# Optimization experiments

Hardware: AMD Instinct MI355X
Metric: run time of the kernel (lower is better)

The kernel has to match this reference:

```python
import jax, jax.numpy as jnp
import numpy as np

Q, C, T = 256, 128, 128
L = Q + C + T            # 512
D = 1024                 # d_model
H = 8                    # heads
DK = D // H              # 128 = self_attn.d_k
F = 3                    # num_latent_relations
R = 50                   # num_relation_kinds = len(relations2id)
FF = 4 * D               # feed-forward hidden
DEFAULT_QQ_ID = 0        # relations2id['q:q-default']
EPS = 1e-5


def setup_inputs():
    key = jax.random.key(0)
    ks = jax.random.split(key, 40)
    s = 0.02
    def nrm(k, shape, scale=s):
        return jax.random.normal(k, shape, jnp.float32) * scale
    inp = {
        'x': jax.random.normal(ks[0], (1, L, D), jnp.float32),
        'qc_relation': jax.random.uniform(ks[1], (Q, C, F), jnp.float32),
        'cq_relation': jax.random.uniform(ks[2], (C, Q, F), jnp.float32),
        'qt_relation': jax.random.uniform(ks[3], (Q, T, F), jnp.float32),
        'tq_relation': jax.random.uniform(ks[4], (T, Q, F), jnp.float32),
        'ct_relation': jax.random.randint(ks[5], (C + T, C + T), 0, R, jnp.int32),
        'predefined_relation': jax.random.randint(ks[6], (L, L), 0, R, jnp.int32),
        'mask': jnp.ones((1, L, L), jnp.int32),
        # relation embedding tables
        'rel_k_emb': nrm(ks[7], (R, DK)), 'rel_v_emb': nrm(ks[8], (R, DK)),
        'lqc_k': nrm(ks[9], (F, DK)), 'lqc_v': nrm(ks[10], (F, DK)),
        'lcq_k': nrm(ks[11], (F, DK)), 'lcq_v': nrm(ks[12], (F, DK)),
        'lqt_k': nrm(ks[13], (F, DK)), 'lqt_v': nrm(ks[14], (F, DK)),
        'ltq_k': nrm(ks[15], (F, DK)), 'ltq_v': nrm(ks[16], (F, DK)),
        # attention projections (torch Linear: y = x @ W.T + b)
        'Wq': nrm(ks[17], (D, D)), 'bq': jnp.zeros((D,), jnp.float32),
        'Wk': nrm(ks[18], (D, D)), 'bk': jnp.zeros((D,), jnp.float32),
        'Wv': nrm(ks[19], (D, D)), 'bv': jnp.zeros((D,), jnp.float32),
        'Wo': nrm(ks[20], (D, D)), 'bo': jnp.zeros((D,), jnp.float32),
        # layer norms
        'ln1_g': jnp.ones((D,), jnp.float32), 'ln1_b': jnp.zeros((D,), jnp.float32),
        'ln2_g': jnp.ones((D,), jnp.float32), 'ln2_b': jnp.zeros((D,), jnp.float32),
        # FFN
        'W1': nrm(ks[21], (FF, D)), 'b1': jnp.zeros((FF,), jnp.float32),
        'W2': nrm(ks[22], (D, FF)), 'b2': jnp.zeros((D,), jnp.float32),
    }
    return inp


def layer_norm(x, g, b):
    m = jnp.mean(x, -1, keepdims=True)
    v = jnp.mean((x - m) ** 2, -1, keepdims=True)
    return (x - m) * jax.lax.rsqrt(v + EPS) * g + b


def build_latent_relation(ct, qc, cq, qt, tq, emb, lqc, lcq, lqt, ltq):
    # qq block: every entry is the default-qq embedding row
    qq = jnp.broadcast_to(emb[DEFAULT_QQ_ID], (Q, Q, DK))
    qc_e = jnp.einsum('qcf,fd->qcd', qc, lqc)
    cq_e = jnp.einsum('cqf,fd->cqd', cq, lcq)
    qt_e = jnp.einsum('qtf,fd->qtd', qt, lqt)
    tq_e = jnp.einsum('tqf,fd->tqd', tq, ltq)
    ct_e = emb[ct]                                      # [(c+t),(c+t),DK]
    top = jnp.concatenate([qq, qc_e, qt_e], axis=1)      # [Q, L, DK]
    bot = jnp.concatenate([jnp.concatenate([cq_e, tq_e], 0), ct_e], axis=1)  # [C+T, L, DK]
    return jnp.concatenate([top, bot], axis=0)           # [L, L, DK]


def relation_attention(x, rel_k, rel_v, mask, Wq, bq, Wk, bk, Wv, bv, Wo, bo):
    B = x.shape[0]
    def proj(W, b):
        return (x @ W.T + b).reshape(B, L, H, DK).transpose(0, 2, 1, 3)  # [B,H,L,DK]
    q, k, v = proj(Wq, bq), proj(Wk, bk), proj(Wv, bv)
    scores = (jnp.einsum('bhid,bhjd->bhij', q, k)
              + jnp.einsum('bhid,ijd->bhij', q, rel_k)) / jnp.sqrt(jnp.float32(DK))
    scores = jnp.where(mask[:, None] == 0, jnp.float32(-1e9), scores)
    p = jax.nn.softmax(scores, axis=-1)
    o = (jnp.einsum('bhij,bhjd->bhid', p, v)
         + jnp.einsum('bhij,ijd->bhid', p, rel_v))
    o = o.transpose(0, 2, 1, 3).reshape(B, L, D)
    return o @ Wo.T + bo


def reference(x, qc_relation, cq_relation, qt_relation, tq_relation,
              ct_relation, predefined_relation, mask,
              rel_k_emb, rel_v_emb, lqc_k, lqc_v, lcq_k, lcq_v,
              lqt_k, lqt_v, ltq_k, ltq_v,
              Wq, bq, Wk, bk, Wv, bv, Wo, bo,
              ln1_g, ln1_b, ln2_g, ln2_b, W1, b1, W2, b2):
    # latent relation build + combine with predefined lookup
    rel_k = (rel_k_emb[predefined_relation]
             + build_latent_relation(ct_relation, qc_relation, cq_relation,
                                     qt_relation, tq_relation,
                                     rel_k_emb, lqc_k, lcq_k, lqt_k, ltq_k))
    rel_v = (rel_v_emb[predefined_relation]
             + build_latent_relation(ct_relation, qc_relation, cq_relation,
                                     qt_relation, tq_relation,
                                     rel_v_emb, lqc_v, lcq_v, lqt_v, ltq_v))
    # sublayer 0: pre-norm relation-biased self attention (dropout=0)
    h = x + relation_attention(layer_norm(x, ln1_g, ln1_b), rel_k, rel_v, mask,
                               Wq, bq, Wk, bk, Wv, bv, Wo, bo)
    # sublayer 1: pre-norm FFN
    y = layer_norm(h, ln2_g, ln2_b)
    ffn = jax.nn.relu(y @ W1.T + b1) @ W2.T + b2
    return h + ffn
```

## Files before the change

### kernel.cpp

```cpp
#include <hip/hip_runtime.h>
#include <hip/hip_bf16.h>

#define LL 512
#define DD 1024
#define HH 8
#define DKK 128
#define QQ 256
#define CCC 128
#define TTT 128
#define RR 50
#define FFF 4096
#define KLD 576
#define SLD 576
#define PLD 1152

typedef __attribute__((ext_vector_type(8))) short short8;
typedef __attribute__((ext_vector_type(4))) float float4v;

__device__ __forceinline__ unsigned short f2bu(float f) {
  __hip_bfloat16 h = __float2bfloat16(f);
  unsigned short u; __builtin_memcpy(&u, &h, 2); return u;
}
__device__ __forceinline__ float b2f(unsigned short u) {
  unsigned int v = ((unsigned int)u) << 16;
  float f; __builtin_memcpy(&f, &v, 4); return f;
}
__device__ __forceinline__ int4 cvt8(float4 x, float4 y) {
  int4 o;
  o.x = (int)f2bu(x.x) | ((int)f2bu(x.y) << 16);
  o.y = (int)f2bu(x.z) | ((int)f2bu(x.w) << 16);
  o.z = (int)f2bu(y.x) | ((int)f2bu(y.y) << 16);
  o.w = (int)f2bu(y.z) | ((int)f2bu(y.w) << 16);
  return o;
}

__device__ __forceinline__ void lds_barrier() {
  __builtin_amdgcn_sched_barrier(0);
  __builtin_amdgcn_s_waitcnt(0xC07F);
  __builtin_amdgcn_s_barrier();
  __builtin_amdgcn_sched_barrier(0);
}

#define LOADSET(A0,A1,B0,B1,F0,F1,F2,F3,itv) { int k0v = (itv) << 6;          \
  A0 = *(const int4*)(Az + (size_t)(bm + r)*lda + k0v + gc*8);                \
  A1 = *(const int4*)(Az + (size_t)(bm + 32 + r)*lda + k0v + gc*8);           \
  if constexpr (!CONVB) {                                                     \
    B0 = *(const int4*)(Bz16 + (size_t)(bnb + r)*ldb + k0v + gc*8);           \
    if constexpr (NB > 1)                                                     \
      B1 = *(const int4*)(Bz16 + (size_t)(bnb + 32 + r)*ldb + k0v + gc*8);    \
  } else {                                                                    \
    F0 = *(const float4*)(Bz32 + (size_t)(bnb + r)*ldb + k0v + gc*8);         \
    F1 = *(const float4*)(Bz32 + (size_t)(bnb + r)*ldb + k0v + gc*8 + 4);     \
    if constexpr (NB > 1) {                                                   \
      F2 = *(const float4*)(Bz32 + (size_t)(bnb + 32 + r)*ldb + k0v + gc*8);  \
      F3 = *(const float4*)(Bz32 + (size_t)(bnb + 32 + r)*ldb + k0v + gc*8 + 4); } } }

#define STORESET2(basep,A0,A1,B0,B1,F0,F1,F2,F3) {                            \
  char* bse = (basep);                                                        \
  *(int4*)(bse + r*128 + sl*16) = A0;                                         \
  *(int4*)(bse + (32 + r)*128 + sl*16) = A1;                                  \
  if constexpr (!CONVB) {                                                     \
    *(int4*)(bse + ABYTES + r*128 + sl*16) = B0;                              \
    if constexpr (NB > 1)                                                     \
      *(int4*)(bse + ABYTES + (32 + r)*128 + sl*16) = B1;                     \
  } else {                                                                    \
    *(int4*)(bse + ABYTES + r*128 + sl*16) = cvt8(F0, F1);                    \
    if constexpr (NB > 1)                                                     \
      *(int4*)(bse + ABYTES + (32 + r)*128 + sl*16) = cvt8(F2, F3); } }

__global__ __launch_bounds__(256) void kprep_kernel(
    const float* __restrict__ embk,
    const float* __restrict__ lqc, const float* __restrict__ lqt,
    const float* __restrict__ lcq, const float* __restrict__ ltq,
    unsigned short* __restrict__ Kh)
{
  int g = blockIdx.x*256 + threadIdx.x;
  if (g >= 8*64*128) return;
  int d = g & 127, rr = (g >> 7) & 63, h = g >> 13;
  float v = 0.f;
  if (rr < 50) v = embk[rr*128 + d];
  else if (rr < 62) {
    int u = rr - 50; int tb = u/3, f = u - tb*3;
    const float* tab = (tb==0) ? lqc : (tb==1) ? lqt : (tb==2) ? lcq : ltq;
    v = tab[f*128 + d];
  }
  Kh[((size_t)h*KLD + 512 + rr)*DKK + d] = f2bu(v);
}

__global__ __launch_bounds__(256) void ln_bf16_kernel(const float* __restrict__ x,
    const float* __restrict__ g, const float* __restrict__ b,
    unsigned short* __restrict__ y)
{
  int row = blockIdx.x, t = threadIdx.x;
  const float4 xv = ((const float4*)(x + row*DD))[t];
  float s  = xv.x+xv.y+xv.z+xv.w;
  float ss = xv.x*xv.x+xv.y*xv.y+xv.z*xv.z+xv.w*xv.w;
  __shared__ float rs[256], rss[256];
  rs[t]=s; rss[t]=ss; __syncthreads();
  for (int st=128; st>0; st>>=1){ if (t<st){ rs[t]+=rs[t+st]; rss[t]+=rss[t+st]; } __syncthreads(); }
  float mean = rs[0] * (1.0f/DD);
  float var  = rss[0]*(1.0f/DD) - mean*mean;
  float inv  = rsqrtf(var + 1e-5f);
  float4 gv = ((const float4*)g)[t], bv = ((const float4*)b)[t];
  ushort4 ov;
  ov.x = f2bu((xv.x-mean)*inv*gv.x + bv.x);
  ov.y = f2bu((xv.y-mean)*inv*gv.y + bv.y);
  ov.z = f2bu((xv.z-mean)*inv*gv.z + bv.z);
  ov.w = f2bu((xv.w-mean)*inv*gv.w + bv.w);
  ((ushort4*)(y + row*DD))[t] = ov;
}

__global__ __launch_bounds__(256) void ln_bf16_addb_kernel(float* __restrict__ x,
    const float* __restrict__ g, const float* __restrict__ b,
    const float* __restrict__ b2, unsigned short* __restrict__ y)
{
  int row = blockIdx.x, t = threadIdx.x;
  const float4 xv = ((const float4*)(x + row*DD))[t];
  float s  = xv.x+xv.y+xv.z+xv.w;
  float ss = xv.x*xv.x+xv.y*xv.y+xv.z*xv.z+xv.w*xv.w;
  __shared__ float rs[256], rss[256];
  rs[t]=s; rss[t]=ss; __syncthreads();
  for (int st=128; st>0; st>>=1){ if (t<st){ rs[t]+=rs[t+st]; rss[t]+=rss[t+st]; } __syncthreads(); }
  float mean = rs[0] * (1.0f/DD);
  float var  = rss[0]*(1.0f/DD) - mean*mean;
  float inv  = rsqrtf(var + 1e-5f);
  float4 gv = ((const float4*)g)[t], bv = ((const float4*)b)[t];
  ushort4 ov;
  ov.x = f2bu((xv.x-mean)*inv*gv.x + bv.x);
  ov.y = f2bu((xv.y-mean)*inv*gv.y + bv.y);
  ov.z = f2bu((xv.z-mean)*inv*gv.z + bv.z);
  ov.w = f2bu((xv.w-mean)*inv*gv.w + bv.w);
  ((ushort4*)(y + row*DD))[t] = ov;
  float4 b2v = ((const float4*)b2)[t];
  float4 nx; nx.x = xv.x+b2v.x; nx.y = xv.y+b2v.y; nx.z = xv.z+b2v.z; nx.w = xv.w+b2v.w;
  ((float4*)(x + row*DD))[t] = nx;
}

template<int BN, int DEPTH, int CONVB, int ZK, int OUT_BF16, int RELU, int HAS_SRC, int HAS_BIAS>
__global__ __launch_bounds__(256) void gemm_pl(
    const unsigned short* __restrict__ A, int lda, size_t sAz,
    const void* __restrict__ Bv, int ldb, size_t sBz,
    const float* __restrict__ bias,
    const float* __restrict__ src, int ldsrc, size_t sSz,
    void* __restrict__ Cv, int ldc, size_t sCz,
    int K)
{
  constexpr int BM = 64;
  constexpr int WM = 32, WN = BN/2, FM = 2, FN = WN/16;
  constexpr int NB = BN/32;
  constexpr int ABYTES = BM*128, TILE = ABYTES + BN*128;
  __shared__ char lds[2*TILE];
  int t = threadIdx.x, w = t >> 6, l = t & 63;
  size_t z = blockIdx.z;
  const unsigned short* Az = A + z*sAz;
  const unsigned short* Bz16 = (const unsigned short*)Bv + (CONVB ? 0 : z*sBz);
  const float*          Bz32 = (const float*)Bv + (CONVB ? z*sBz : 0);
  int bm = blockIdx.y*BM, bn = blockIdx.x*BN;
  int bnb = bn;
  int wm = (w>>1)*WM, wn = (w&1)*WN;

  float4v acc[FM][FN];
  #pragma unroll
  for (int m=0;m<FM;++m)
    #pragma unroll
    for (int n=0;n<FN;++n) acc[m][n] = (float4v){0.f,0.f,0.f,0.f};

  int r = t >> 3, sl = t & 7;
  int gc = sl ^ (r & 7);
  int quad = l >> 4, lrow = l & 15;
  const int nit = K >> 6;

  int4 Aa0, Aa1, Ab0, Ab1;  float4 Af0, Af1, Af2, Af3;
  int4 Ba0, Ba1, Bb0, Bb1;  float4 Bf0, Bf1, Bf2, Bf3;
  int4 Ca0, Ca1, Cb0, Cb1;  float4 Cf0, Cf1, Cf2, Cf3;
  int4 Da0, Da1, Db0, Db1;  float4 Df0, Df1, Df2, Df3;

  auto compute = [&](const char* base) {
    const char* ab = base;
    const char* bb = base + ABYTES;
    #pragma unroll
    for (int step=0; step<2; ++step) {
      int c = step*4 + quad;
      short8 af[FM], bf[FN];
      #pragma unroll
      for (int m=0;m<FM;++m) {
        int Rw = wm + m*16 + lrow;
        af[m] = *(const short8*)(ab + Rw*128 + ((c ^ (Rw & 7))*16));
      }
      #pragma unroll
      for (int n=0;n<FN;++n) {
        int Rw = wn + n*16 + lrow;
        bf[n] = *(const short8*)(bb + Rw*128 + ((c ^ (Rw & 7))*16));
      }
      #pragma unroll
      for (int m=0;m<FM;++m)
        #pragma unroll
        for (int n=0;n<FN;++n)
          acc[m][n] = __builtin_amdgcn_mfma_f32_16x16x32_bf16(af[m], bf[n], acc[m][n], 0, 0, 0);
    }
  };

  if constexpr (DEPTH == 2) {
    LOADSET(Aa0,Aa1,Ab0,Ab1,Af0,Af1,Af2,Af3, 0);
    LOADSET(Ba0,Ba1,Bb0,Bb1,Bf0,Bf1,Bf2,Bf3, 1);
    for (int it = 0; it < nit; it += 2) {
      STORESET2(lds, Aa0,Aa1,Ab0,Ab1,Af0,Af1,Af2,Af3);
      if (it + 2 < nit) LOADSET(Aa0,Aa1,Ab0,Ab1,Af0,Af1,Af2,Af3, it+2);
      lds_barrier();
      compute(lds);
      STORESET2(lds + TILE, Ba0,Ba1,Bb0,Bb1,Bf0,Bf1,Bf2,Bf3);
      if (it + 3 < nit) LOADSET(Ba0,Ba1,Bb0,Bb1,Bf0,Bf1,Bf2,Bf3, it+3);
      lds_barrier();
      compute(lds + TILE);
    }
  } else {
    LOADSET(Aa0,Aa1,Ab0,Ab1,Af0,Af1,Af2,Af3, 0);
    LOADSET(Ba0,Ba1,Bb0,Bb1,Bf0,Bf1,Bf2,Bf3, 1);
    LOADSET(Ca0,Ca1,Cb0,Cb1,Cf0,Cf1,Cf2,Cf3, 2);
    LOADSET(Da0,Da1,Db0,Db1,Df0,Df1,Df2,Df3, 3);
    for (int it = 0; it < nit; it += 4) {
      STORESET2(lds, Aa0,Aa1,Ab0,Ab1,Af0,Af1,Af2,Af3);
      if (it + 4 < nit) LOADSET(Aa0,Aa1,Ab0,Ab1,Af0,Af1,Af2,Af3, it+4);
      lds_barrier();
      compute(lds);
      STORESET2(lds + TILE, Ba0,Ba1,Bb0,Bb1,Bf0,Bf1,Bf2,Bf3);
      if (it + 5 < nit) LOADSET(Ba0,Ba1,Bb0,Bb1,Bf0,Bf1,Bf2,Bf3, it+5);
      lds_barrier();
      compute(lds + TILE);
      STORESET2(lds, Ca0,Ca1,Cb0,Cb1,Cf0,Cf1,Cf2,Cf3);
      if (it + 6 < nit) LOADSET(Ca0,Ca1,Cb0,Cb1,Cf0,Cf1,Cf2,Cf3, it+6);
      lds_barrier();
      compute(lds);
      STORESET2(lds + TILE, Da0,Da1,Db0,Db1,Df0,Df1,Df2,Df3);
      if (it + 7 < nit) LOADSET(Da0,Da1,Db0,Db1,Df0,Df1,Df2,Df3, it+7);
      lds_barrier();
      compute(lds + TILE);
    }
  }

  #pragma unroll
  for (int m=0;m<FM;++m)
    #pragma unroll
    for (int n=0;n<FN;++n)
      #pragma unroll
      for (int rg=0;rg<4;++rg) {
        int row = bm + wm + m*16 + quad*4 + rg;
        int col = bn + wn + n*16 + lrow;
        float vv = acc[m][n][rg];
        if (ZK) {
          atomicAdd(&((float*)Cv)[(size_t)row*ldc + col], vv);
        } else {
          if (HAS_BIAS) vv += bias[col];
          if (HAS_SRC)  vv += src[z*sSz + (size_t)row*ldsrc + col];
          if (RELU) vv = fmaxf(vv, 0.f);
          if (OUT_BF16) ((unsigned short*)Cv)[z*sCz + (size_t)row*ldc + col] = f2bu(vv);
          else          ((float*)Cv)[z*sCz + (size_t)row*ldc + col] = vv;
        }
      }
}

__global__ __launch_bounds__(256) void gemm_qkv_pl(
    const unsigned short* __restrict__ A,
    const float* __restrict__ Wq, const float* __restrict__ Wk,
    const float* __restrict__ Wv,
    const float* __restrict__ bq, const float* __restrict__ bk,
    const float* __restrict__ bv,
    unsigned short* __restrict__ Qh, unsigned short* __restrict__ Kh,
    unsigned short* __restrict__ Vt)
{
  constexpr int BN = 64, CONVB = 1;
  constexpr int WM = 32, WN = 32, FM = 2, FN = 2;
  constexpr int NB = 2;
  constexpr int ABYTES = 64*128, TILE = ABYTES + BN*128;
  __shared__ char lds[2*TILE];
  int t = threadIdx.x, w = t >> 6, l = t & 63;
  int bm = blockIdx.y*64, bn = blockIdx.x*BN;
  int wm = (w>>1)*WM, wn = (w&1)*WN;
  const int lda = DD, ldb = DD, nit = DD >> 6;
  const unsigned short* Az = A;
  int part0 = bn >> 10;
  const float* Bz32 = (part0==0 ? Wq : part0==1 ? Wk : Wv) + (size_t)(bn & 1023)*DD;
  const unsigned short* Bz16 = nullptr; (void)Bz16;
  int bnb = 0;

  float4v acc[FM][FN];
  #pragma unroll
  for (int m=0;m<FM;++m)
    #pragma unroll
    for (int n=0;n<FN;++n) acc[m][n] = (float4v){0.f,0.f,0.f,0.f};

  int r = t >> 3, sl = t & 7;
  int gc = sl ^ (r & 7);
  int quad = l >> 4, lrow = l & 15;

  int4 Aa0, Aa1, Ab0, Ab1;  float4 Af0, Af1, Af2, Af3;
  int4 Ba0, Ba1, Bb0, Bb1;  float4 Bf0, Bf1, Bf2, Bf3;
  int4 Ca0, Ca1, Cb0, Cb1;  float4 Cf0, Cf1, Cf2, Cf3;
  int4 Da0, Da1, Db0, Db1;  float4 Df0, Df1, Df2, Df3;

  auto compute = [&](const char* base) {
    const char* ab = base;
    const char* bb = base + ABYTES;
    #pragma unroll
    for (int step=0; step<2; ++step) {
      int c = step*4 + quad;
      short8 af[FM], bf[FN];
      #pragma unroll
      for (int m=0;m<FM;++m) {
        int Rw = wm + m*16 + lrow;
        af[m] = *(const short8*)(ab + Rw*128 + ((c ^ (Rw & 7))*16));
      }
      #pragma unroll
      for (int n=0;n<FN;++n) {
        int Rw = wn + n*16 + lrow;
        bf[n] = *(const short8*)(bb + Rw*128 + ((c ^ (Rw & 7))*16));
      }
      #pragma unroll
      for (int m=0;m<FM;++m)
        #pragma unroll
        for (int n=0;n<FN;++n)
          acc[m][n] = __builtin_amdgcn_mfma_f32_16x16x32_bf16(af[m], bf[n], acc[m][n], 0, 0, 0);
    }
  };

  LOADSET(Aa0,Aa1,Ab0,Ab1,Af0,Af1,Af2,Af3, 0);
  LOADSET(Ba0,Ba1,Bb0,Bb1,Bf0,Bf1,Bf2,Bf3, 1);
  LOADSET(Ca0,Ca1,Cb0,Cb1,Cf0,Cf1,Cf2,Cf3, 2);
  LOADSET(Da0,Da1,Db0,Db1,Df0,Df1,Df2,Df3, 3);
  for (int it = 0; it < nit; it += 4) {
    STORESET2(lds, Aa0,Aa1,Ab0,Ab1,Af0,Af1,Af2,Af3);
    if (it + 4 < nit) LOADSET(Aa0,Aa1,Ab0,Ab1,Af0,Af1,Af2,Af3, it+4);
    lds_barrier();
    compute(lds);
    STORESET2(lds + TILE, Ba0,Ba1,Bb0,Bb1,Bf0,Bf1,Bf2,Bf3);
    if (it + 5 < nit) LOADSET(Ba0,Ba1,Bb0,Bb1,Bf0,Bf1,Bf2,Bf3, it+5);
    lds_barrier();
    compute(lds + TILE);
    STORESET2(lds, Ca0,Ca1,Cb0,Cb1,Cf0,Cf1,Cf2,Cf3);
    if (it + 6 < nit) LOADSET(Ca0,Ca1,Cb0,Cb1,Cf0,Cf1,Cf2,Cf3, it+6);
    lds_barrier();
    compute(lds);
    STORESET2(lds + TILE, Da0,Da1,Db0,Db1,Df0,Df1,Df2,Df3);
    if (it + 7 < nit) LOADSET(Da0,Da1,Db0,Db1,Df0,Df1,Df2,Df3, it+7);
    lds_barrier();
    compute(lds + TILE);
  }

  #pragma unroll
  for (int m=0;m<FM;++m)
    #pragma unroll
    for (int n=0;n<FN;++n)
      #pragma unroll
      for (int rg=0;rg<4;++rg) {
        int row = bm + wm + m*16 + quad*4 + rg;
        int col = bn + wn + n*16 + lrow;
        int part = col >> 10, hh = (col >> 7) & 7, d = col & 127;
        const float* bp = (part==0) ? bq : (part==1) ? bk : bv;
        float vv = acc[m][n][rg] + bp[col & 1023];
        unsigned short o = f2bu(vv);
        if (part == 0)      Qh[((size_t)hh*LL + row)*DKK + d] = o;
        else if (part == 1) Kh[((size_t)hh*KLD + row)*DKK + d] = o;
        else                Vt[((size_t)hh*DKK + d)*LL + row] = o;
      }
}

__global__ __launch_bounds__(512) void softmax_pw_kernel(
    float* __restrict__ S,
    const float* __restrict__ qcr, const float* __restrict__ cqr,
    const float* __restrict__ qtr, const float* __restrict__ tqr,
    const int* __restrict__ ct,   const int* __restrict__ pred,
    const int* __restrict__ mask,
    const float* __restrict__ embv,
    const float* __restrict__ lqc_v, const float* __restrict__ lcq_v,
    const float* __restrict__ lqt_v, const float* __restrict__ ltq_v,
    float* __restrict__ o2)
{
  int i = blockIdx.x, j = threadIdx.x, w = j >> 6;
  __shared__ float qerow8[8][52];
  __shared__ float lq1s[8][3], lq2s[8][3];
  __shared__ float pws[8][52];
  __shared__ float pf1s[8][3], pf2s[8][3];
  __shared__ float redm[8][8], reds[8][8];

  for (int k = j; k < 8*52; k += 512) ((float*)pws)[k] = 0.f;
  if (j < 24) { ((float*)pf1s)[j] = 0.f; ((float*)pf2s)[j] = 0.f; }
  if (j < 400) {
    int h = j / 50, rr = j - h*50;
    qerow8[h][rr] = S[((size_t)(h*LL + i))*SLD + 512 + rr];
  } else if (j >= 448 && j < 472) {
    int u = j - 448; int h = u / 3, f = u - h*3;
    int base = (i < QQ) ? 562 : (i < QQ+CCC) ? 568 : 571;
    lq1s[h][f] = S[((size_t)(h*LL + i))*SLD + base + f];
    lq2s[h][f] = (i < QQ) ? S[((size_t)(h*LL + i))*SLD + 565 + f] : 0.f;
  }

  int predv = pred[i*LL + j];
  int maskv = mask[i*LL + j];
  float c0=0.f, c1=0.f, c2=0.f; int route; int scat2 = 0;
  if (i < QQ) {
    if (j < QQ) { route = 0; scat2 = 0; }
    else if (j < QQ+CCC) { const float* rr = qcr + (i*CCC + (j-QQ))*3;
      c0=rr[0]; c1=rr[1]; c2=rr[2]; route = 1; }
    else { const float* rr = qtr + (i*TTT + (j-QQ-CCC))*3;
      c0=rr[0]; c1=rr[1]; c2=rr[2]; route = 2; }
  } else {
    if (j < QQ) { const float* rr = (i < QQ+CCC) ? cqr + ((i-QQ)*QQ + j)*3
                                                 : tqr + ((i-QQ-CCC)*QQ + j)*3;
      c0=rr[0]; c1=rr[1]; c2=rr[2]; route = 1; }
    else { route = 0; scat2 = ct[(i-QQ)*(CCC+TTT) + (j-QQ)]; }
  }

  float sv[8];
  #pragma unroll
  for (int h=0; h<8; ++h) sv[h] = S[((size_t)(h*LL + i))*SLD + j];
  __syncthreads();

  #pragma unroll
  for (int h=0; h<8; ++h) {
    float s = sv[h] + qerow8[h][predv];
    if (route == 0)      s += qerow8[h][scat2];
    else if (route == 1) s += c0*lq1s[h][0] + c1*lq1s[h][1] + c2*lq1s[h][2];
    else                 s += c0*lq2s[h][0] + c1*lq2s[h][1] + c2*lq2s[h][2];
    s *= 0.08838834764831845f;
    if (maskv == 0) s = -1e9f;
    sv[h] = s;
  }

  float mv[8];
  #pragma unroll
  for (int h=0; h<8; ++h) mv[h] = sv[h];
  #pragma unroll
  for (int off=32; off>=1; off>>=1) {
    #pragma unroll
    for (int h=0; h<8; ++h) mv[h] = fmaxf(mv[h], __shfl_xor(mv[h], off));
  }
  if ((j & 63) == 0) {
    #pragma unroll
    for (int h=0; h<8; ++h) redm[h][w] = mv[h];
  }
  __syncthreads();
  float ev[8];
  #pragma unroll
  for (int h=0; h<8; ++h) {
    float mx = redm[h][0];
    #pragma unroll
    for (int k=1; k<8; ++k) mx = fmaxf(mx, redm[h][k]);
    ev[h] = __expf(sv[h] - mx);
  }
  float sm[8];
  #pragma unroll
  for (int h=0; h<8; ++h) sm[h] = ev[h];
  #pragma unroll
  for (int off=32; off>=1; off>>=1) {
    #pragma unroll
    for (int h=0; h<8; ++h) sm[h] += __shfl_xor(sm[h], off);
  }
  if ((j & 63) == 0) {
    #pragma unroll
    for (int h=0; h<8; ++h) reds[h][w] = sm[h];
  }
  __syncthreads();
  float pv[8];
  #pragma unroll
  for (int h=0; h<8; ++h) {
    float tot = 0.f;
    #pragma unroll
    for (int k=0; k<8; ++k) tot += reds[h][k];
    pv[h] = ev[h] * (1.0f/tot);
    ((unsigned short*)S)[((size_t)(h*LL + i))*PLD + j] = f2bu(pv[h]);
    atomicAdd(&pws[h][predv], pv[h]);
    if (route == 0) atomicAdd(&pws[h][scat2], pv[h]);
  }
  if (route == 1) {
    #pragma unroll
    for (int h=0; h<8; ++h) {
      float f0 = pv[h]*c0, f1 = pv[h]*c1, f2 = pv[h]*c2;
      #pragma unroll
      for (int off=32; off>=1; off>>=1) {
        f0 += __shfl_xor(f0, off); f1 += __shfl_xor(f1, off); f2 += __shfl_xor(f2, off);
      }
      if ((j & 63) == 0) {
        atomicAdd(&pf1s[h][0], f0); atomicAdd(&pf1s[h][1], f1); atomicAdd(&pf1s[h][2], f2);
      }
    }
  } else if (route == 2) {
    #pragma unroll
    for (int h=0; h<8; ++h) {
      float f0 = pv[h]*c0, f1 = pv[h]*c1, f2 = pv[h]*c2;
      #pragma unroll
      for (int off=32; off>=1; off>>=1) {
        f0 += __shfl_xor(f0, off); f1 += __shfl_xor(f1, off); f2 += __shfl_xor(f2, off);
      }
      if ((j & 63) == 0) {
        atomicAdd(&pf2s[h][0], f0); atomicAdd(&pf2s[h][1], f1); atomicAdd(&pf2s[h][2], f2);
      }
    }
  }
  __syncthreads();

  {
    int h0 = j >> 7;
    int d  = j & 127;
    const float* tab1; const float* tab2 = nullptr;
    if (i < QQ)          { tab1 = lqc_v; tab2 = lqt_v; }
    else if (i < QQ+CCC) { tab1 = lcq_v; }
    else                 { tab1 = ltq_v; }
    float accA = 0.f, accB = 0.f;
    #pragma unroll 5
    for (int rr = 0; rr < RR; ++rr) {
      float evv = embv[rr*128 + d];
      accA += pws[h0][rr]*evv; accB += pws[h0+4][rr]*evv;
    }
    float t0 = tab1[d], t1 = tab1[128+d], t2 = tab1[256+d];
    accA += pf1s[h0][0]*t0 + pf1s[h0][1]*t1 + pf1s[h0][2]*t2;
    accB += pf1s[h0+4][0]*t0 + pf1s[h0+4][1]*t1 + pf1s[h0+4][2]*t2;
    if (tab2) {
      float u0 = tab2[d], u1 = tab2[128+d], u2 = tab2[256+d];
      accA += pf2s[h0][0]*u0 + pf2s[h0][1]*u1 + pf2s[h0][2]*u2;
      accB += pf2s[h0+4][0]*u0 + pf2s[h0+4][1]*u1 + pf2s[h0+4][2]*u2;
    }
    o2[((size_t)(h0*LL) + i)*DKK + d] = accA;
    o2[((size_t)((h0+4)*LL) + i)*DKK + d] = accB;
  }
}

extern "C" void kernel_launch(void* const* d_in, const int* in_sizes, int n_in,
                              void* d_out, int out_size, void* d_ws, size_t ws_size,
                              hipStream_t stream)
{
  const float* x    = (const float*)d_in[0];
  const float* qcr  = (const float*)d_in[1];
  const float* cqr  = (const float*)d_in[2];
  const float* qtr  = (const float*)d_in[3];
  const float* tqr  = (const float*)d_in[4];
  const int*   ct   = (const int*)d_in[5];
  const int*   pred = (const int*)d_in[6];
  const int*   mask = (const int*)d_in[7];
  const float* embk = (const float*)d_in[8];
  const float* embv = (const float*)d_in[9];
  const float* lqc_k = (const float*)d_in[10];
  const float* lqc_v = (const float*)d_in[11];
  const float* lcq_k = (const float*)d_in[12];
  const float* lcq_v = (const float*)d_in[13];
  const float* lqt_k = (const float*)d_in[14];
  const float* lqt_v = (const float*)d_in[15];
  const float* ltq_k = (const float*)d_in[16];
  const float* ltq_v = (const float*)d_in[17];
  const float* Wq = (const float*)d_in[18]; const float* bq = (const float*)d_in[19];
  const float* Wk = (const float*)d_in[20]; const float* bk = (const float*)d_in[21];
  const float* Wv = (const float*)d_in[22]; const float* bv = (const float*)d_in[23];
  const float* Wo = (const float*)d_in[24]; const float* bo = (const float*)d_in[25];
  const float* ln1_g = (const float*)d_in[26]; const float* ln1_b = (const float*)d_in[27];
  const float* ln2_g = (const float*)d_in[28]; const float* ln2_b = (const float*)d_in[29];
  const float* W1 = (const float*)d_in[30]; const float* b1 = (const float*)d_in[31];
  const float* W2 = (const float*)d_in[32]; const float* b2 = (const float*)d_in[33];
  float* out = (float*)d_out;

  float* wsf = (float*)d_ws;
  float* S    = wsf;
  float* o2   = S + (size_t)HH*LL*SLD;
  unsigned short* ub = (unsigned short*)(o2 + (size_t)HH*LL*DKK);
  unsigned short* ybuf_b = ub;
  unsigned short* obuf_b = ybuf_b + LL*DD;
  unsigned short* Qh     = obuf_b + LL*DD;
  unsigned short* Kh     = Qh + (size_t)HH*LL*DKK;
  unsigned short* Vt     = Kh + (size_t)HH*KLD*DKK;
  unsigned short* PS     = (unsigned short*)S;
  unsigned short* hidden = (unsigned short*)S;

  kprep_kernel<<<(8*64*128 + 255)/256, 256, 0, stream>>>(
      embk, lqc_k, lqt_k, lcq_k, ltq_k, Kh);
  ln_bf16_kernel<<<LL, 256, 0, stream>>>(x, ln1_g, ln1_b, ybuf_b);
  gemm_qkv_pl<<<dim3(48, 8), 256, 0, stream>>>(ybuf_b, Wq, Wk, Wv, bq, bk, bv,
                                               Qh, Kh, Vt);
  gemm_pl<64,2,0,0,0,0,0,0><<<dim3(9, 8, 8), 256, 0, stream>>>(
      Qh, DKK, (size_t)LL*DKK, Kh, DKK, (size_t)KLD*DKK,
      nullptr, nullptr, 0, 0, S, SLD, (size_t)LL*SLD, DKK);
  softmax_pw_kernel<<<LL, 512, 0, stream>>>(
      S, qcr, cqr, qtr, tqr, ct, pred, mask,
      embv, lqc_v, lcq_v, lqt_v, ltq_v, o2);
  gemm_pl<32,4,0,0,1,0,1,0><<<dim3(4, 8, 8), 256, 0, stream>>>(
      PS, PLD, (size_t)LL*PLD, Vt, LL, (size_t)DKK*LL,
      nullptr, o2, DKK, (size_t)LL*DKK, obuf_b, DD, (size_t)DKK, LL);
  gemm_pl<32,4,1,0,0,0,1,1><<<dim3(32, 8, 1), 256, 0, stream>>>(
      obuf_b, DD, 0, Wo, DD, 0, bo, x, DD, 0, out, DD, 0, DD);
  ln_bf16_addb_kernel<<<LL, 256, 0, stream>>>(out, ln2_g, ln2_b, b2, ybuf_b);
  gemm_pl<64,4,1,0,1,1,0,1><<<dim3(64, 8, 1), 256, 0, stream>>>(
      ybuf_b, DD, 0, W1, DD, 0, b1, nullptr, 0, 0, hidden, FFF, 0, DD);
  gemm_pl<64,4,1,1,0,0,0,0><<<dim3(16, 8, 4), 256, 0, stream>>>(
      hidden, FFF, (size_t)1024, W2, FFF, (size_t)1024,
      nullptr, nullptr, 0, 0, out, DD, 0, 1024);
}
```

Before: 251.8 us.

## Fuse QK^T, relation-biased softmax, and PV into one attention kernel

Replaces three launches (QK^T GEMM, softmax with relation scatter, PV GEMM) with a single kernel. Each block handles 16 query rows of one head, computes the scores into LDS with MFMA, applies the relation biases and softmax, and accumulates the relation-value terms. It then multiplies P by V from LDS and writes bf16 output directly. This removes the global round-trips for S, P and o2 plus two launches, but the grid is only 256 blocks with large LDS use, which may lower occupancy.

```diff
diff --git a/kernel.cpp b/kernel.cpp
--- a/kernel.cpp
+++ b/kernel.cpp
@@ -12,7 +12,6 @@
 #define FFF 4096
 #define KLD 576
 #define SLD 576
-#define PLD 1152
 
 typedef __attribute__((ext_vector_type(8))) short short8;
 typedef __attribute__((ext_vector_type(4))) float float4v;
@@ -364,163 +363,229 @@
       }
 }
 
-__global__ __launch_bounds__(512) void softmax_pw_kernel(
-    float* __restrict__ S,
+#define AT_QROWB 272
+#define AT_KROWB 272
+#define AT_SROW  584
+#define AT_PROWB 1040
+#define AT_VROWB 144
+#define AT_OFF_KT 4352
+#define AT_OFF_S  21760
+#define AT_OFF_V  21760
+#define AT_OFF_PW 59136
+#define AT_OFF_PF1 62464
+#define AT_OFF_PF2 62720
+#define AT_LDS 62976
+
+__global__ __launch_bounds__(256) void attn_fused(
+    const unsigned short* __restrict__ Qh, const unsigned short* __restrict__ Kh,
+    const unsigned short* __restrict__ Vt,
     const float* __restrict__ qcr, const float* __restrict__ cqr,
     const float* __restrict__ qtr, const float* __restrict__ tqr,
-    const int* __restrict__ ct,   const int* __restrict__ pred,
+    const int* __restrict__ ct, const int* __restrict__ pred,
     const int* __restrict__ mask,
-    const float* __restrict__ embv,
-    const float* __restrict__ lqc_v, const float* __restrict__ lcq_v,
-    const float* __restrict__ lqt_v, const float* __restrict__ ltq_v,
-    float* __restrict__ o2)
+    const float* __restrict__ embv, const float* __restrict__ lqc_v,
+    const float* __restrict__ lcq_v, const float* __restrict__ lqt_v,
+    const float* __restrict__ ltq_v,
+    unsigned short* __restrict__ obuf)
 {
-  int i = blockIdx.x, j = threadIdx.x, w = j >> 6;
-  __shared__ float qerow8[8][52];
-  __shared__ float lq1s[8][3], lq2s[8][3];
-  __shared__ float pws[8][52];
-  __shared__ float pf1s[8][3], pf2s[8][3];
-  __shared__ float redm[8][8], reds[8][8];
-
-  for (int k = j; k < 8*52; k += 512) ((float*)pws)[k] = 0.f;
-  if (j < 24) { ((float*)pf1s)[j] = 0.f; ((float*)pf2s)[j] = 0.f; }
-  if (j < 400) {
-    int h = j / 50, rr = j - h*50;
-    qerow8[h][rr] = S[((size_t)(h*LL + i))*SLD + 512 + rr];
-  } else if (j >= 448 && j < 472) {
-    int u = j - 448; int h = u / 3, f = u - h*3;
-    int base = (i < QQ) ? 562 : (i < QQ+CCC) ? 568 : 571;
-    lq1s[h][f] = S[((size_t)(h*LL + i))*SLD + base + f];
-    lq2s[h][f] = (i < QQ) ? S[((size_t)(h*LL + i))*SLD + 565 + f] : 0.f;
-  }
-
-  int predv = pred[i*LL + j];
-  int maskv = mask[i*LL + j];
-  float c0=0.f, c1=0.f, c2=0.f; int route; int scat2 = 0;
-  if (i < QQ) {
-    if (j < QQ) { route = 0; scat2 = 0; }
-    else if (j < QQ+CCC) { const float* rr = qcr + (i*CCC + (j-QQ))*3;
-      c0=rr[0]; c1=rr[1]; c2=rr[2]; route = 1; }
-    else { const float* rr = qtr + (i*TTT + (j-QQ-CCC))*3;
-      c0=rr[0]; c1=rr[1]; c2=rr[2]; route = 2; }
-  } else {
-    if (j < QQ) { const float* rr = (i < QQ+CCC) ? cqr + ((i-QQ)*QQ + j)*3
-                                                 : tqr + ((i-QQ-CCC)*QQ + j)*3;
-      c0=rr[0]; c1=rr[1]; c2=rr[2]; route = 1; }
-    else { route = 0; scat2 = ct[(i-QQ)*(CCC+TTT) + (j-QQ)]; }
-  }
-
-  float sv[8];
-  #pragma unroll
-  for (int h=0; h<8; ++h) sv[h] = S[((size_t)(h*LL + i))*SLD + j];
-  __syncthreads();
-
-  #pragma unroll
-  for (int h=0; h<8; ++h) {
-    float s = sv[h] + qerow8[h][predv];
-    if (route == 0)      s += qerow8[h][scat2];
-    else if (route == 1) s += c0*lq1s[h][0] + c1*lq1s[h][1] + c2*lq1s[h][2];
-    else                 s += c0*lq2s[h][0] + c1*lq2s[h][1] + c2*lq2s[h][2];
+  __shared__ __align__(16) char lds[AT_LDS];
+  const int t = threadIdx.x;
+  const int w = t >> 6, l = t & 63, quad = l >> 4, lrow = l & 15;
+  const int i0 = blockIdx.x * 16, h = blockIdx.y;
+
+  for (int k2 = t; k2 < 960; k2 += 256) ((float*)(lds + AT_OFF_PW))[k2] = 0.f;
+
+  {
+    int qr = t >> 4, qc = t & 15;
+    *(int4*)(lds + qr*AT_QROWB + qc*16) =
+        *(const int4*)(Qh + ((size_t)h*LL + i0 + qr)*DKK + qc*8);
+  }
+
+  const int kr = t >> 4, kc = t & 15;
+  int4 kv0, kv1, kv2, kv3;
+#define AT_LOADK(jtv) { size_t kb = (size_t)h*KLD + (size_t)(jtv)*64 + kr;     \
+    kv0 = *(const int4*)(Kh + (kb     )*DKK + kc*8);                           \
+    kv1 = *(const int4*)(Kh + (kb + 16)*DKK + kc*8);                           \
+    kv2 = *(const int4*)(Kh + (kb + 32)*DKK + kc*8);                           \
+    kv3 = *(const int4*)(Kh + (kb + 48)*DKK + kc*8); }
+#define AT_STOREK() {                                                          \
+    *(int4*)(lds + AT_OFF_KT + (kr     )*AT_KROWB + kc*16) = kv0;              \
+    *(int4*)(lds + AT_OFF_KT + (kr + 16)*AT_KROWB + kc*16) = kv1;              \
+    *(int4*)(lds + AT_OFF_KT + (kr + 32)*AT_KROWB + kc*16) = kv2;              \
+    *(int4*)(lds + AT_OFF_KT + (kr + 48)*AT_KROWB + kc*16) = kv3; }
+
+  AT_LOADK(0);
+  for (int jt = 0; jt < 9; ++jt) {
+    lds_barrier();
+    AT_STOREK();
+    if (jt + 1 < 9) AT_LOADK(jt + 1);
+    lds_barrier();
+    float4v acc = (float4v){0.f,0.f,0.f,0.f};
+    #pragma unroll
+    for (int kk = 0; kk < 4; ++kk) {
+      int c = kk*4 + quad;
+      short8 af = *(const short8*)(lds + lrow*AT_QROWB + c*16);
+      short8 bf = *(const short8*)(lds + AT_OFF_KT + (w*16 + lrow)*AT_KROWB + c*16);
+      acc = __builtin_amdgcn_mfma_f32_16x16x32_bf16(af, bf, acc, 0, 0, 0);
+    }
+    #pragma unroll
+    for (int rg = 0; rg < 4; ++rg)
+      ((float*)(lds + AT_OFF_S))[(quad*4 + rg)*AT_SROW + jt*64 + w*16 + lrow] = acc[rg];
+  }
+  lds_barrier();
+
+  const int row = t >> 4, l16 = t & 15;
+  const int i = i0 + row;
+  const float* Srow = (const float*)(lds + AT_OFF_S) + row*AT_SROW;
+  const int base = (i0 < QQ) ? 562 : (i0 < QQ + CCC) ? 568 : 571;
+  const float lq1a = Srow[base], lq1b = Srow[base+1], lq1c = Srow[base+2];
+  const float lq2a = Srow[565], lq2b = Srow[566], lq2c = Srow[567];
+
+  const int vr = t >> 3, vc = t & 7;
+  int4 vv0, vv1, vv2, vv3;
+#define AT_LOADV(itv) { size_t vb = (size_t)h*DKK + vr;                        \
+    size_t vo = (size_t)(itv)*64 + vc*8;                                       \
+    vv0 = *(const int4*)(Vt + (vb      )*LL + vo);                             \
+    vv1 = *(const int4*)(Vt + (vb + 32)*LL + vo);                              \
+    vv2 = *(const int4*)(Vt + (vb + 64)*LL + vo);                              \
+    vv3 = *(const int4*)(Vt + (vb + 96)*LL + vo); }
+#define AT_STOREV() {                                                          \
+    *(int4*)(lds + AT_OFF_V + (vr     )*AT_VROWB + vc*16) = vv0;               \
+    *(int4*)(lds + AT_OFF_V + (vr + 32)*AT_VROWB + vc*16) = vv1;               \
+    *(int4*)(lds + AT_OFF_V + (vr + 64)*AT_VROWB + vc*16) = vv2;               \
+    *(int4*)(lds + AT_OFF_V + (vr + 96)*AT_VROWB + vc*16) = vv3; }
+  AT_LOADV(0);
+
+  float sv[32];
+  #pragma unroll
+  for (int m = 0; m < 32; ++m) {
+    int j = m*16 + l16;
+    int predv = pred[i*LL + j];
+    int maskv = mask[i*LL + j];
+    float s = Srow[j] + Srow[512 + predv];
+    if (i0 < QQ) {
+      if (j < QQ) s += Srow[512];
+      else if (j < QQ + CCC) {
+        const float* r3 = qcr + ((size_t)i*CCC + (j - QQ))*3;
+        s += r3[0]*lq1a + r3[1]*lq1b + r3[2]*lq1c;
+      } else {
+        const float* r3 = qtr + ((size_t)i*TTT + (j - QQ - CCC))*3;
+        s += r3[0]*lq2a + r3[1]*lq2b + r3[2]*lq2c;
+      }
+    } else {
+      if (j < QQ) {
+        const float* r3 = (i < QQ + CCC) ? cqr + ((size_t)(i - QQ)*QQ + j)*3
+                                         : tqr + ((size_t)(i - QQ - CCC)*QQ + j)*3;
+        s += r3[0]*lq1a + r3[1]*lq1b + r3[2]*lq1c;
+      } else {
+        int scat2 = ct[(i - QQ)*(CCC + TTT) + (j - QQ)];
+        s += Srow[512 + scat2];
+      }
+    }
     s *= 0.08838834764831845f;
     if (maskv == 0) s = -1e9f;
-    sv[h] = s;
-  }
-
-  float mv[8];
-  #pragma unroll
-  for (int h=0; h<8; ++h) mv[h] = sv[h];
-  #pragma unroll
-  for (int off=32; off>=1; off>>=1) {
-    #pragma unroll
-    for (int h=0; h<8; ++h) mv[h] = fmaxf(mv[h], __shfl_xor(mv[h], off));
-  }
-  if ((j & 63) == 0) {
-    #pragma unroll
-    for (int h=0; h<8; ++h) redm[h][w] = mv[h];
-  }
-  __syncthreads();
-  float ev[8];
-  #pragma unroll
-  for (int h=0; h<8; ++h) {
-    float mx = redm[h][0];
-    #pragma unroll
-    for (int k=1; k<8; ++k) mx = fmaxf(mx, redm[h][k]);
-    ev[h] = __expf(sv[h] - mx);
-  }
-  float sm[8];
-  #pragma unroll
-  for (int h=0; h<8; ++h) sm[h] = ev[h];
-  #pragma unroll
-  for (int off=32; off>=1; off>>=1) {
-    #pragma unroll
-    for (int h=0; h<8; ++h) sm[h] += __shfl_xor(sm[h], off);
-  }
-  if ((j & 63) == 0) {
-    #pragma unroll
-    for (int h=0; h<8; ++h) reds[h][w] = sm[h];
-  }
-  __syncthreads();
-  float pv[8];
-  #pragma unroll
-  for (int h=0; h<8; ++h) {
-    float tot = 0.f;
-    #pragma unroll
-    for (int k=0; k<8; ++k) tot += reds[h][k];
-    pv[h] = ev[h] * (1.0f/tot);
-    ((unsigned short*)S)[((size_t)(h*LL + i))*PLD + j] = f2bu(pv[h]);
-    atomicAdd(&pws[h][predv], pv[h]);
-    if (route == 0) atomicAdd(&pws[h][scat2], pv[h]);
-  }
-  if (route == 1) {
-    #pragma unroll
-    for (int h=0; h<8; ++h) {
-      float f0 = pv[h]*c0, f1 = pv[h]*c1, f2 = pv[h]*c2;
-      #pragma unroll
-      for (int off=32; off>=1; off>>=1) {
-        f0 += __shfl_xor(f0, off); f1 += __shfl_xor(f1, off); f2 += __shfl_xor(f2, off);
-      }
-      if ((j & 63) == 0) {
-        atomicAdd(&pf1s[h][0], f0); atomicAdd(&pf1s[h][1], f1); atomicAdd(&pf1s[h][2], f2);
-      }
-    }
-  } else if (route == 2) {
-    #pragma unroll
-    for (int h=0; h<8; ++h) {
-      float f0 = pv[h]*c0, f1 = pv[h]*c1, f2 = pv[h]*c2;
-      #pragma unroll
-      for (int off=32; off>=1; off>>=1) {
-        f0 += __shfl_xor(f0, off); f1 += __shfl_xor(f1, off); f2 += __shfl_xor(f2, off);
-      }
-      if ((j & 63) == 0) {
-        atomicAdd(&pf2s[h][0], f0); atomicAdd(&pf2s[h][1], f1); atomicAdd(&pf2s[h][2], f2);
-      }
-    }
-  }
-  __syncthreads();
-
-  {
-    int h0 = j >> 7;
-    int d  = j & 127;
-    const float* tab1; const float* tab2 = nullptr;
-    if (i < QQ)          { tab1 = lqc_v; tab2 = lqt_v; }
-    else if (i < QQ+CCC) { tab1 = lcq_v; }
-    else                 { tab1 = ltq_v; }
-    float accA = 0.f, accB = 0.f;
+    sv[m] = s;
+  }
+  float mx = sv[0];
+  #pragma unroll
+  for (int m = 1; m < 32; ++m) mx = fmaxf(mx, sv[m]);
+  #pragma unroll
+  for (int off = 8; off >= 1; off >>= 1) mx = fmaxf(mx, __shfl_xor(mx, off));
+  float sum = 0.f;
+  #pragma unroll
+  for (int m = 0; m < 32; ++m) { float e = __expf(sv[m] - mx); sv[m] = e; sum += e; }
+  #pragma unroll
+  for (int off = 8; off >= 1; off >>= 1) sum += __shfl_xor(sum, off);
+  const float inv = 1.0f / sum;
+
+  float f0=0.f, f1=0.f, f2=0.f, g0=0.f, g1=0.f, g2=0.f;
+  #pragma unroll
+  for (int m = 0; m < 32; ++m) {
+    int j = m*16 + l16;
+    float p = sv[m] * inv;
+    *(unsigned short*)(lds + row*AT_PROWB + j*2) = f2bu(p);
+    int predv = pred[i*LL + j];
+    atomicAdd((float*)(lds + AT_OFF_PW) + row*52 + predv, p);
+    if (i0 < QQ) {
+      if (j < QQ) atomicAdd((float*)(lds + AT_OFF_PW) + row*52, p);
+      else if (j < QQ + CCC) {
+        const float* r3 = qcr + ((size_t)i*CCC + (j - QQ))*3;
+        f0 += p*r3[0]; f1 += p*r3[1]; f2 += p*r3[2];
+      } else {
+        const float* r3 = qtr + ((size_t)i*TTT + (j - QQ - CCC))*3;
+        g0 += p*r3[0]; g1 += p*r3[1]; g2 += p*r3[2];
+      }
+    } else {
+      if (j < QQ) {
+        const float* r3 = (i < QQ + CCC) ? cqr + ((size_t)(i - QQ)*QQ + j)*3
+                                         : tqr + ((size_t)(i - QQ - CCC)*QQ + j)*3;
+        f0 += p*r3[0]; f1 += p*r3[1]; f2 += p*r3[2];
+      } else {
+        int scat2 = ct[(i - QQ)*(CCC + TTT) + (j - QQ)];
+        atomicAdd((float*)(lds + AT_OFF_PW) + row*52 + scat2, p);
+      }
+    }
+  }
+  #pragma unroll
+  for (int off = 8; off >= 1; off >>= 1) {
+    f0 += __shfl_xor(f0, off); f1 += __shfl_xor(f1, off); f2 += __shfl_xor(f2, off);
+    g0 += __shfl_xor(g0, off); g1 += __shfl_xor(g1, off); g2 += __shfl_xor(g2, off);
+  }
+  if (l16 == 0) {
+    float* pf1 = (float*)(lds + AT_OFF_PF1) + row*4;
+    float* pf2 = (float*)(lds + AT_OFF_PF2) + row*4;
+    pf1[0] = f0; pf1[1] = f1; pf1[2] = f2;
+    pf2[0] = g0; pf2[1] = g1; pf2[2] = g2;
+  }
+
+  float4v oacc0 = (float4v){0.f,0.f,0.f,0.f};
+  float4v oacc1 = (float4v){0.f,0.f,0.f,0.f};
+  for (int it = 0; it < 8; ++it) {
+    lds_barrier();
+    AT_STOREV();
+    if (it + 1 < 8) AT_LOADV(it + 1);
+    lds_barrier();
+    #pragma unroll
+    for (int kk = 0; kk < 2; ++kk) {
+      int c = kk*4 + quad;
+      short8 pa = *(const short8*)(lds + lrow*AT_PROWB + it*128 + c*16);
+      short8 vf0 = *(const short8*)(lds + AT_OFF_V + (w*32 + lrow)*AT_VROWB + c*16);
+      short8 vf1 = *(const short8*)(lds + AT_OFF_V + (w*32 + 16 + lrow)*AT_VROWB + c*16);
+      oacc0 = __builtin_amdgcn_mfma_f32_16x16x32_bf16(pa, vf0, oacc0, 0, 0, 0);
+      oacc1 = __builtin_amdgcn_mfma_f32_16x16x32_bf16(pa, vf1, oacc1, 0, 0, 0);
+    }
+  }
+
+  const float* tab1 = (i0 < QQ) ? lqc_v : (i0 < QQ + CCC) ? lcq_v : ltq_v;
+  const bool hasT2 = (i0 < QQ);
+  const float* pws = (const float*)(lds + AT_OFF_PW);
+  #pragma unroll
+  for (int n = 0; n < 2; ++n) {
+    int d = w*32 + n*16 + lrow;
+    float a0=0.f, a1=0.f, a2=0.f, a3=0.f;
     #pragma unroll 5
     for (int rr = 0; rr < RR; ++rr) {
-      float evv = embv[rr*128 + d];
-      accA += pws[h0][rr]*evv; accB += pws[h0+4][rr]*evv;
-    }
-    float t0 = tab1[d], t1 = tab1[128+d], t2 = tab1[256+d];
-    accA += pf1s[h0][0]*t0 + pf1s[h0][1]*t1 + pf1s[h0][2]*t2;
-    accB += pf1s[h0+4][0]*t0 + pf1s[h0+4][1]*t1 + pf1s[h0+4][2]*t2;
-    if (tab2) {
-      float u0 = tab2[d], u1 = tab2[128+d], u2 = tab2[256+d];
-      accA += pf2s[h0][0]*u0 + pf2s[h0][1]*u1 + pf2s[h0][2]*u2;
-      accB += pf2s[h0+4][0]*u0 + pf2s[h0+4][1]*u1 + pf2s[h0+4][2]*u2;
-    }
-    o2[((size_t)(h0*LL) + i)*DKK + d] = accA;
-    o2[((size_t)((h0+4)*LL) + i)*DKK + d] = accB;
+      float evv = embv[rr*DKK + d];
+      a0 += pws[(quad*4+0)*52 + rr]*evv;
+      a1 += pws[(quad*4+1)*52 + rr]*evv;
+      a2 += pws[(quad*4+2)*52 + rr]*evv;
+      a3 += pws[(quad*4+3)*52 + rr]*evv;
+    }
+    float t0 = tab1[d], t1 = tab1[DKK + d], t2 = tab1[2*DKK + d];
+    float u0 = 0.f, u1 = 0.f, u2 = 0.f;
+    if (hasT2) { u0 = lqt_v[d]; u1 = lqt_v[DKK + d]; u2 = lqt_v[2*DKK + d]; }
+    #pragma unroll
+    for (int rg = 0; rg < 4; ++rg) {
+      int rw = quad*4 + rg;
+      const float* pf1 = (const float*)(lds + AT_OFF_PF1) + rw*4;
+      const float* pf2 = (const float*)(lds + AT_OFF_PF2) + rw*4;
+      float aval = (rg==0) ? a0 : (rg==1) ? a1 : (rg==2) ? a2 : a3;
+      float oval = (n==0) ? oacc0[rg] : oacc1[rg];
+      float val = oval + aval
+                + pf1[0]*t0 + pf1[1]*t1 + pf1[2]*t2
+                + pf2[0]*u0 + pf2[1]*u1 + pf2[2]*u2;
+      obuf[(size_t)(i0 + rw)*DD + h*DKK + d] = f2bu(val);
+    }
   }
 }
 
@@ -565,7 +630,6 @@
   unsigned short* Qh     = obuf_b + LL*DD;
   unsigned short* Kh     = Qh + (size_t)HH*LL*DKK;
   unsigned short* Vt     = Kh + (size_t)HH*KLD*DKK;
-  unsigned short* PS     = (unsigned short*)S;
   unsigned short* hidden = (unsigned short*)S;
 
   kprep_kernel<<<(8*64*128 + 255)/256, 256, 0, stream>>>(
@@ -573,15 +637,9 @@
   ln_bf16_kernel<<<LL, 256, 0, stream>>>(x, ln1_g, ln1_b, ybuf_b);
   gemm_qkv_pl<<<dim3(48, 8), 256, 0, stream>>>(ybuf_b, Wq, Wk, Wv, bq, bk, bv,
                                                Qh, Kh, Vt);
-  gemm_pl<64,2,0,0,0,0,0,0><<<dim3(9, 8, 8), 256, 0, stream>>>(
-      Qh, DKK, (size_t)LL*DKK, Kh, DKK, (size_t)KLD*DKK,
-      nullptr, nullptr, 0, 0, S, SLD, (size_t)LL*SLD, DKK);
-  softmax_pw_kernel<<<LL, 512, 0, stream>>>(
-      S, qcr, cqr, qtr, tqr, ct, pred, mask,
-      embv, lqc_v, lcq_v, lqt_v, ltq_v, o2);
-  gemm_pl<32,4,0,0,1,0,1,0><<<dim3(4, 8, 8), 256, 0, stream>>>(
-      PS, PLD, (size_t)LL*PLD, Vt, LL, (size_t)DKK*LL,
-      nullptr, o2, DKK, (size_t)LL*DKK, obuf_b, DD, (size_t)DKK, LL);
+  attn_fused<<<dim3(32, 8), 256, 0, stream>>>(
+      Qh, Kh, Vt, qcr, cqr, qtr, tqr, ct, pred, mask,
+      embv, lqc_v, lcq_v, lqt_v, ltq_v, obuf_b);
   gemm_pl<32,4,1,0,0,0,1,1><<<dim3(32, 8, 1), 256, 0, stream>>>(
       obuf_b, DD, 0, Wo, DD, 0, bo, x, DD, 0, out, DD, 0, DD);
   ln_bf16_addb_kernel<<<LL, 256, 0, stream>>>(out, ln2_g, ln2_b, b2, ybuf_b);
```

Measured after the change: 249.5 us. Within noise of the previous version (-0.9%).
